# Kernel optimization log

Hardware: AMD Instinct MI355X
Metric: run time of the kernel (lower is better)

Reference implementation:

```python
import jax, jax.numpy as jnp
import numpy as np

HEADS = 16
DIM_HEAD = 64
EPS = 1e-5

def layer_norm(x, g, b):
    mu = jnp.mean(x, axis=-1, keepdims=True)
    var = jnp.mean(jnp.square(x - mu), axis=-1, keepdims=True)
    return (x - mu) * jax.lax.rsqrt(var + EPS) * g + b

def setup_inputs() -> dict:
    key = jax.random.key(0)
    ks = jax.random.split(key, 8)
    b, n_t, n_a = 4, 1024, 1024
    text_dim, audio_dim = 1024, 1024
    inner = HEADS * DIM_HEAD  # 1024
    s_in = 1.0 / np.sqrt(audio_dim)
    return {
        "text": jax.random.normal(ks[0], (b, n_t, text_dim), jnp.float32),
        "audio": jax.random.normal(ks[1], (b, n_a, audio_dim), jnp.float32),
        "g_text": jnp.ones((text_dim,), jnp.float32),
        "b_text": jnp.zeros((text_dim,), jnp.float32),
        "g_audio": jnp.ones((audio_dim,), jnp.float32),
        "b_audio": jnp.zeros((audio_dim,), jnp.float32),
        "W_qk": jax.random.normal(ks[2], (audio_dim, inner), jnp.float32) * s_in,
        "W_v": jax.random.normal(ks[3], (text_dim, inner), jnp.float32) * s_in,
        "W_out": jax.random.normal(ks[4], (inner, audio_dim), jnp.float32) * s_in,
        "b_out": jnp.zeros((audio_dim,), jnp.float32),
        "W_th": jax.random.normal(ks[5], (HEADS, HEADS), jnp.float32) / np.sqrt(HEADS),
    }

def reference(text, audio, g_text, b_text, g_audio, b_audio, W_qk, W_v, W_out, b_out, W_th):
    b = audio.shape[0]
    scale = DIM_HEAD ** -0.5
    text = layer_norm(text, g_text, b_text)
    audio = layer_norm(audio, g_audio, b_audio)
    # projections; qk acts as query, v acts as BOTH key and value
    qk = (audio @ W_qk).reshape(b, -1, HEADS, DIM_HEAD).transpose(0, 2, 1, 3)  # b h i d
    v = (text @ W_v).reshape(b, -1, HEADS, DIM_HEAD).transpose(0, 2, 1, 3)    # b h j d
    sim = jnp.einsum('bhid,bhjd->bhij', qk, v) * scale
    attn = jax.nn.softmax(sim, axis=-1)
    # talking-heads: 1x1 conv over head dim == mixing matrix over h
    attn = jnp.einsum('hg,bgij->bhij', W_th, attn)
    out = jnp.einsum('bhij,bhjd->bhid', attn, v)
    out = out.transpose(0, 2, 1, 3).reshape(b, -1, HEADS * DIM_HEAD)
    return out @ W_out + b_out
```

## Files before the change

kernel.cpp:

```cpp
#include <hip/hip_runtime.h>

typedef unsigned short u16;
typedef __bf16 bf16x8 __attribute__((ext_vector_type(8)));
typedef float f32x4 __attribute__((ext_vector_type(4)));
typedef unsigned short u16x4 __attribute__((ext_vector_type(4)));

static __device__ __forceinline__ u16 f2bf(float f){
  __bf16 h = (__bf16)f;
  return __builtin_bit_cast(u16, h);
}

#define MFMA(a,b,c) __builtin_amdgcn_mfma_f32_16x16x32_bf16(a,b,c,0,0,0)

__global__ __launch_bounds__(256) void ln_rows(const float* __restrict__ x,
    const float* __restrict__ g, const float* __restrict__ bta, u16* __restrict__ y)
{
  const int row = blockIdx.x;
  const int t = threadIdx.x;
  const float4 xv = ((const float4*)(x + (size_t)row*1024))[t];
  float s  = xv.x+xv.y+xv.z+xv.w;
  float sq = xv.x*xv.x+xv.y*xv.y+xv.z*xv.z+xv.w*xv.w;
  #pragma unroll
  for (int off=32; off; off>>=1){ s += __shfl_xor(s,off); sq += __shfl_xor(sq,off); }
  __shared__ float red[8];
  const int wid = t>>6, lane = t&63;
  if (lane==0){ red[wid]=s; red[4+wid]=sq; }
  __syncthreads();
  s  = red[0]+red[1]+red[2]+red[3];
  sq = red[4]+red[5]+red[6]+red[7];
  const float mu = s*(1.0f/1024.0f);
  float var = sq*(1.0f/1024.0f) - mu*mu;
  var = fmaxf(var, 0.0f);
  const float rs = rsqrtf(var + 1e-5f);
  const float4 gv = ((const float4*)g)[t];
  const float4 bv = ((const float4*)bta)[t];
  u16x4 o;
  o[0] = f2bf((xv.x-mu)*rs*gv.x + bv.x);
  o[1] = f2bf((xv.y-mu)*rs*gv.y + bv.y);
  o[2] = f2bf((xv.z-mu)*rs*gv.z + bv.z);
  o[3] = f2bf((xv.w-mu)*rs*gv.w + bv.w);
  ((u16x4*)(y + (size_t)row*1024))[t] = o;
}

__global__ __launch_bounds__(256) void transpose_w(const float* __restrict__ W, u16* __restrict__ WT)
{
  __shared__ float tile[32][33];
  const int tid = threadIdx.x;
  const int r0 = blockIdx.y*32, c0 = blockIdx.x*32;
  #pragma unroll
  for (int i=0;i<4;++i){
    int idx = i*256+tid; int r = idx>>5, c = idx&31;
    tile[r][c] = W[(size_t)(r0+r)*1024 + c0+c];
  }
  __syncthreads();
  #pragma unroll
  for (int i=0;i<4;++i){
    int idx = i*256+tid; int r = idx>>5, c = idx&31;
    WT[(size_t)(c0+r)*1024 + r0+c] = f2bf(tile[c][r]);
  }
}

__global__ __launch_bounds__(256) void transpose_v(const u16* __restrict__ V, u16* __restrict__ VT)
{
  __shared__ u16 tile[32][33];
  const int tid = threadIdx.x;
  const size_t base = (size_t)blockIdx.z * 1048576;
  const int r0 = blockIdx.y*32, c0 = blockIdx.x*32;
  #pragma unroll
  for (int i=0;i<4;++i){
    int idx = i*256+tid; int r = idx>>5, c = idx&31;
    tile[r][c] = V[base + (size_t)(r0+r)*1024 + c0+c];
  }
  __syncthreads();
  #pragma unroll
  for (int i=0;i<4;++i){
    int idx = i*256+tid; int r = idx>>5, c = idx&31;
    VT[base + (size_t)(c0+r)*1024 + r0+c] = tile[c][r];
  }
}

__global__ __launch_bounds__(256) void gemm_bt(const u16* __restrict__ A,
    const u16* __restrict__ Bt, u16* __restrict__ Cb, float* __restrict__ Cf,
    const float* __restrict__ bias, int outf)
{
  __shared__ u16 As[128][72];
  __shared__ u16 Bs[128][72];
  const int tid = threadIdx.x, lane = tid&63, wid = tid>>6;
  const int l15 = lane&15, l4 = lane>>4;
  const int m0 = blockIdx.y*128, n0 = blockIdx.x*128;
  const int wr = wid>>1, wc = wid&1;
  const int srow = tid>>3, scol = (tid&7)*8;
  const u16* Ag = A  + (size_t)(m0+srow)*1024 + scol;
  const u16* Bg = Bt + (size_t)(n0+srow)*1024 + scol;
  f32x4 acc[4][4];
  #pragma unroll
  for (int mt=0;mt<4;++mt)
    #pragma unroll
    for (int nt=0;nt<4;++nt) acc[mt][nt] = f32x4{0,0,0,0};

  for (int kt=0; kt<16; ++kt){
    const int k0 = kt*64;
    #pragma unroll
    for (int it=0; it<4; ++it){
      *(bf16x8*)&As[srow+it*32][scol] = *(const bf16x8*)(Ag + (size_t)it*32*1024 + k0);
      *(bf16x8*)&Bs[srow+it*32][scol] = *(const bf16x8*)(Bg + (size_t)it*32*1024 + k0);
    }
    __syncthreads();
    #pragma unroll
    for (int kk=0; kk<2; ++kk){
      bf16x8 af[4], bfv[4];
      #pragma unroll
      for (int mt=0;mt<4;++mt) af[mt]  = *(const bf16x8*)&As[wr*64+mt*16+l15][kk*32+8*l4];
      #pragma unroll
      for (int nt=0;nt<4;++nt) bfv[nt] = *(const bf16x8*)&Bs[wc*64+nt*16+l15][kk*32+8*l4];
      #pragma unroll
      for (int mt=0;mt<4;++mt)
        #pragma unroll
        for (int nt=0;nt<4;++nt)
          acc[mt][nt] = MFMA(af[mt], bfv[nt], acc[mt][nt]);
    }
    __syncthreads();
  }
  #pragma unroll
  for (int mt=0;mt<4;++mt)
    #pragma unroll
    for (int nt=0;nt<4;++nt)
      #pragma unroll
      for (int r=0;r<4;++r){
        const int row = m0 + wr*64+mt*16+l4*4+r;
        const int col = n0 + wc*64+nt*16+l15;
        if (outf) Cf[(size_t)row*1024+col] = acc[mt][nt][r] + bias[col];
        else      Cb[(size_t)row*1024+col] = f2bf(acc[mt][nt][r]);
      }
}

__global__ __launch_bounds__(256) void attn_stats(const u16* __restrict__ qk,
    const u16* __restrict__ v, float* __restrict__ m_arr, float* __restrict__ l_arr)
{
  const int lane = threadIdx.x & 63, wid = threadIdx.x >> 6;
  const int l15 = lane&15, l4 = lane>>4;
  const int b = blockIdx.z, g = blockIdx.y;
  const int i_base = blockIdx.x*64 + wid*16;
  const u16* qrow = qk + (size_t)(b*1024 + i_base + l15)*1024 + g*64 + 8*l4;
  const bf16x8 a0 = *(const bf16x8*)(qrow);
  const bf16x8 a1 = *(const bf16x8*)(qrow + 32);
  float mx[4] = {-1e30f,-1e30f,-1e30f,-1e30f};
  float sm[4] = {0.f,0.f,0.f,0.f};
  const u16* vbase = v + (size_t)(b*1024 + l15)*1024 + g*64 + 8*l4;
  for (int jt=0; jt<64; ++jt){
    const u16* vrow = vbase + (size_t)jt*16*1024;
    f32x4 c = {0,0,0,0};
    c = MFMA(a0, *(const bf16x8*)(vrow),      c);
    c = MFMA(a1, *(const bf16x8*)(vrow + 32), c);
    #pragma unroll
    for (int r=0;r<4;++r){
      const float s = c[r]*0.125f;
      const float nm = fmaxf(mx[r], s);
      sm[r] = sm[r]*__expf(mx[r]-nm) + __expf(s-nm);
      mx[r] = nm;
    }
  }
  #pragma unroll
  for (int r=0;r<4;++r){
    #pragma unroll
    for (int msk=1; msk<16; msk<<=1){
      const float om = __shfl_xor(mx[r], msk);
      const float os = __shfl_xor(sm[r], msk);
      const float nm = fmaxf(mx[r], om);
      sm[r] = sm[r]*__expf(mx[r]-nm) + os*__expf(om-nm);
      mx[r] = nm;
    }
  }
  if (l15 == 0){
    #pragma unroll
    for (int r=0;r<4;++r){
      const int i = i_base + l4*4 + r;
      const size_t idx = (size_t)(b*16+g)*1024 + i;
      m_arr[idx] = mx[r];
      l_arr[idx] = sm[r];
    }
  }
}

__global__ __launch_bounds__(256) void attn_mix_pv(const u16* __restrict__ qk,
    const u16* __restrict__ v, const u16* __restrict__ vt,
    const float* __restrict__ m_arr, const float* __restrict__ l_arr,
    const float* __restrict__ Wth, u16* __restrict__ attn_out)
{
  __shared__ float wth[256];
  __shared__ float P[16][16][36];
  const int tid = threadIdx.x;
  const int lane = tid&63, wid = tid>>6;
  const int l15 = lane&15, l4 = lane>>4;
  const int b = blockIdx.y;
  const int i0 = blockIdx.x*16;
  wth[tid] = Wth[tid];
  float mxs[4][4], ils[4][4];
  #pragma unroll
  for (int gg=0; gg<4; ++gg){
    const int g = wid*4+gg;
    #pragma unroll
    for (int r=0;r<4;++r){
      const size_t idx = (size_t)(b*16+g)*1024 + i0 + l4*4 + r;
      mxs[gg][r] = m_arr[idx];
      ils[gg][r] = 1.0f / l_arr[idx];
    }
  }
  bf16x8 aq[4][2];
  #pragma unroll
  for (int gg=0; gg<4; ++gg){
    const u16* qrow = qk + (size_t)(b*1024 + i0 + l15)*1024 + (wid*4+gg)*64 + 8*l4;
    aq[gg][0] = *(const bf16x8*)(qrow);
    aq[gg][1] = *(const bf16x8*)(qrow + 32);
  }
  f32x4 accO[4][4];
  #pragma unroll
  for (int hh=0;hh<4;++hh)
    #pragma unroll
    for (int dt=0;dt<4;++dt) accO[hh][dt] = f32x4{0,0,0,0};
  __syncthreads();

  for (int jt=0; jt<32; ++jt){
    const int j0 = jt*32;
    #pragma unroll
    for (int gg=0; gg<4; ++gg){
      const int g = wid*4+gg;
      #pragma unroll
      for (int jh=0; jh<2; ++jh){
        const u16* vrow = v + (size_t)(b*1024 + j0 + jh*16 + l15)*1024 + g*64 + 8*l4;
        f32x4 c = {0,0,0,0};
        c = MFMA(aq[gg][0], *(const bf16x8*)(vrow),      c);
        c = MFMA(aq[gg][1], *(const bf16x8*)(vrow + 32), c);
        #pragma unroll
        for (int r=0;r<4;++r){
          const float p = __expf(c[r]*0.125f - mxs[gg][r]) * ils[gg][r];
          P[g][l4*4+r][jh*16+l15] = p;
        }
      }
    }
    __syncthreads();
    float bh[4][8];
    #pragma unroll
    for (int hh=0;hh<4;++hh)
      #pragma unroll
      for (int e=0;e<8;++e) bh[hh][e] = 0.f;
    #pragma unroll
    for (int g2=0; g2<16; ++g2){
      const f32x4 p0 = *(const f32x4*)&P[g2][l15][8*l4];
      const f32x4 p1 = *(const f32x4*)&P[g2][l15][8*l4+4];
      #pragma unroll
      for (int hh=0; hh<4; ++hh){
        const float w = wth[(wid*4+hh)*16+g2];
        #pragma unroll
        for (int e=0;e<4;++e){ bh[hh][e] += w*p0[e]; bh[hh][4+e] += w*p1[e]; }
      }
    }
    #pragma unroll
    for (int hh=0; hh<4; ++hh){
      bf16x8 bfrag;
      #pragma unroll
      for (int e=0;e<8;++e) bfrag[e] = (__bf16)bh[hh][e];
      #pragma unroll
      for (int dt=0; dt<4; ++dt){
        const int c = (wid*4+hh)*64 + dt*16 + l15;
        const u16* vtrow = vt + (size_t)b*1048576 + (size_t)c*1024 + j0 + 8*l4;
        accO[hh][dt] = MFMA(bfrag, *(const bf16x8*)(vtrow), accO[hh][dt]);
      }
    }
    __syncthreads();
  }
  #pragma unroll
  for (int hh=0; hh<4; ++hh)
    #pragma unroll
    for (int dt=0; dt<4; ++dt)
      #pragma unroll
      for (int r=0;r<4;++r){
        const int i = i0 + l4*4 + r;
        const int col = (wid*4+hh)*64 + dt*16 + l15;
        attn_out[(size_t)(b*1024+i)*1024 + col] = f2bf(accO[hh][dt][r]);
      }
}

extern "C" void kernel_launch(void* const* d_in, const int* in_sizes, int n_in,
                              void* d_out, int out_size, void* d_ws, size_t ws_size,
                              hipStream_t stream) {
  const float* text    = (const float*)d_in[0];
  const float* audio   = (const float*)d_in[1];
  const float* g_text  = (const float*)d_in[2];
  const float* b_text  = (const float*)d_in[3];
  const float* g_audio = (const float*)d_in[4];
  const float* b_audio = (const float*)d_in[5];
  const float* W_qk    = (const float*)d_in[6];
  const float* W_v     = (const float*)d_in[7];
  const float* W_out   = (const float*)d_in[8];
  const float* b_out   = (const float*)d_in[9];
  const float* W_th    = (const float*)d_in[10];

  char* ws = (char*)d_ws;
  const size_t MB = 1024*1024;
  u16* text_n  = (u16*)(ws + 0*MB);
  u16* audio_n = (u16*)(ws + 8*MB);
  u16* WqkT    = (u16*)(ws + 16*MB);
  u16* WvT     = (u16*)(ws + 18*MB);
  u16* WoutT   = (u16*)(ws + 20*MB);
  u16* qk      = (u16*)(ws + 22*MB);
  u16* v       = (u16*)(ws + 30*MB);
  u16* vt      = (u16*)(ws + 38*MB);
  float* m_arr = (float*)(ws + 46*MB);
  float* l_arr = (float*)(ws + 47*MB);
  u16* attn_o  = (u16*)(ws + 48*MB);

  transpose_w<<<dim3(32,32), 256, 0, stream>>>(W_qk,  WqkT);
  transpose_w<<<dim3(32,32), 256, 0, stream>>>(W_v,   WvT);
  transpose_w<<<dim3(32,32), 256, 0, stream>>>(W_out, WoutT);
  ln_rows<<<4096, 256, 0, stream>>>(text,  g_text,  b_text,  text_n);
  ln_rows<<<4096, 256, 0, stream>>>(audio, g_audio, b_audio, audio_n);
  gemm_bt<<<dim3(8,32), 256, 0, stream>>>(audio_n, WqkT, qk, nullptr, nullptr, 0);
  gemm_bt<<<dim3(8,32), 256, 0, stream>>>(text_n,  WvT,  v,  nullptr, nullptr, 0);
  transpose_v<<<dim3(32,32,4), 256, 0, stream>>>(v, vt);
  attn_stats<<<dim3(16,16,4), 256, 0, stream>>>(qk, v, m_arr, l_arr);
  attn_mix_pv<<<dim3(64,4), 256, 0, stream>>>(qk, v, vt, m_arr, l_arr, W_th, attn_o);
  gemm_bt<<<dim3(8,32), 256, 0, stream>>>(attn_o, WoutT, nullptr, (float*)d_out, b_out, 1);
}
```

Before: 332.0 us.

## Split attention mix/PV over key chunks with 512-thread blocks and reduction pass

The fused attention-mix/PV kernel now uses 512 threads per block, two heads per wave, and optionally splits the key dimension into four chunks along grid z. Each chunk writes fp32 partial outputs that a new reduce kernel sums and converts to bf16. The goal is more blocks and waves in flight than the original 256-block grid, which underfills the GPU. The cost is extra fp32 partial traffic, an extra launch, and workspace buffers reassigned depending on available workspace size.

```diff
diff --git a/kernel.cpp b/kernel.cpp
--- a/kernel.cpp
+++ b/kernel.cpp
@@ -182,103 +182,106 @@
   }
 }
 
-__global__ __launch_bounds__(256) void attn_mix_pv(const u16* __restrict__ qk,
+__global__ __launch_bounds__(512,4) void attn_mix_pv2(const u16* __restrict__ qk,
     const u16* __restrict__ v, const u16* __restrict__ vt,
     const float* __restrict__ m_arr, const float* __restrict__ l_arr,
-    const float* __restrict__ Wth, u16* __restrict__ attn_out)
+    const float* __restrict__ Wth, float* __restrict__ Upart, int njt)
 {
   __shared__ float wth[256];
   __shared__ float P[16][16][36];
   const int tid = threadIdx.x;
   const int lane = tid&63, wid = tid>>6;
   const int l15 = lane&15, l4 = lane>>4;
-  const int b = blockIdx.y;
+  const int b = blockIdx.y, z = blockIdx.z;
   const int i0 = blockIdx.x*16;
-  wth[tid] = Wth[tid];
-  float mxs[4][4], ils[4][4];
-  #pragma unroll
-  for (int gg=0; gg<4; ++gg){
-    const int g = wid*4+gg;
+  const size_t bb = (size_t)b*1048576;
+  if (tid < 256) wth[tid] = Wth[tid];
+
+  float mxs[2][4], ils[2][4];
+  bf16x8 aq[2][2];
+  #pragma unroll
+  for (int gg=0; gg<2; ++gg){
+    const int g = 2*wid+gg;
     #pragma unroll
     for (int r=0;r<4;++r){
-      const size_t idx = (size_t)(b*16+g)*1024 + i0 + l4*4 + r;
+      const size_t idx = (size_t)(b*16+g)*1024 + i0 + 4*l4 + r;
       mxs[gg][r] = m_arr[idx];
       ils[gg][r] = 1.0f / l_arr[idx];
     }
-  }
-  bf16x8 aq[4][2];
-  #pragma unroll
-  for (int gg=0; gg<4; ++gg){
-    const u16* qrow = qk + (size_t)(b*1024 + i0 + l15)*1024 + (wid*4+gg)*64 + 8*l4;
-    aq[gg][0] = *(const bf16x8*)(qrow);
-    aq[gg][1] = *(const bf16x8*)(qrow + 32);
-  }
-  f32x4 accO[4][4];
-  #pragma unroll
-  for (int hh=0;hh<4;++hh)
-    #pragma unroll
-    for (int dt=0;dt<4;++dt) accO[hh][dt] = f32x4{0,0,0,0};
-  __syncthreads();
-
-  for (int jt=0; jt<32; ++jt){
-    const int j0 = jt*32;
-    #pragma unroll
-    for (int gg=0; gg<4; ++gg){
-      const int g = wid*4+gg;
+    const u16* qrow = qk + bb + (size_t)(i0+l15)*1024 + g*64 + 8*l4;
+    aq[gg][0] = *(const bf16x8*)qrow;
+    aq[gg][1] = *(const bf16x8*)(qrow+32);
+  }
+  f32x4 acc[2][4];
+  #pragma unroll
+  for (int hh=0;hh<2;++hh)
+    #pragma unroll
+    for (int dt=0;dt<4;++dt) acc[hh][dt] = f32x4{0,0,0,0};
+
+  for (int jt=0; jt<njt; ++jt){
+    const int j0 = (z*njt + jt)*32;
+    #pragma unroll
+    for (int gg=0; gg<2; ++gg){
+      const int g = 2*wid+gg;
       #pragma unroll
       for (int jh=0; jh<2; ++jh){
-        const u16* vrow = v + (size_t)(b*1024 + j0 + jh*16 + l15)*1024 + g*64 + 8*l4;
+        const u16* vrow = v + bb + (size_t)(j0 + jh*16 + l15)*1024 + g*64 + 8*l4;
         f32x4 c = {0,0,0,0};
         c = MFMA(aq[gg][0], *(const bf16x8*)(vrow),      c);
         c = MFMA(aq[gg][1], *(const bf16x8*)(vrow + 32), c);
         #pragma unroll
-        for (int r=0;r<4;++r){
-          const float p = __expf(c[r]*0.125f - mxs[gg][r]) * ils[gg][r];
-          P[g][l4*4+r][jh*16+l15] = p;
-        }
+        for (int r=0;r<4;++r)
+          P[g][4*l4+r][jh*16+l15] = __expf(c[r]*0.125f - mxs[gg][r]) * ils[gg][r];
       }
     }
     __syncthreads();
-    float bh[4][8];
-    #pragma unroll
-    for (int hh=0;hh<4;++hh)
-      #pragma unroll
-      for (int e=0;e<8;++e) bh[hh][e] = 0.f;
-    #pragma unroll
-    for (int g2=0; g2<16; ++g2){
-      const f32x4 p0 = *(const f32x4*)&P[g2][l15][8*l4];
-      const f32x4 p1 = *(const f32x4*)&P[g2][l15][8*l4+4];
-      #pragma unroll
-      for (int hh=0; hh<4; ++hh){
-        const float w = wth[(wid*4+hh)*16+g2];
+    #pragma unroll
+    for (int hh=0; hh<2; ++hh){
+      const int h = 2*wid+hh;
+      float bh[8];
+      #pragma unroll
+      for (int e=0;e<8;++e) bh[e] = 0.f;
+      #pragma unroll
+      for (int g2=0; g2<16; ++g2){
+        const f32x4 p0 = *(const f32x4*)&P[g2][l15][8*l4];
+        const f32x4 p1 = *(const f32x4*)&P[g2][l15][8*l4+4];
+        const float w = wth[h*16+g2];
         #pragma unroll
-        for (int e=0;e<4;++e){ bh[hh][e] += w*p0[e]; bh[hh][4+e] += w*p1[e]; }
+        for (int e=0;e<4;++e){ bh[e] += w*p0[e]; bh[4+e] += w*p1[e]; }
       }
-    }
-    #pragma unroll
-    for (int hh=0; hh<4; ++hh){
-      bf16x8 bfrag;
-      #pragma unroll
-      for (int e=0;e<8;++e) bfrag[e] = (__bf16)bh[hh][e];
-      #pragma unroll
-      for (int dt=0; dt<4; ++dt){
-        const int c = (wid*4+hh)*64 + dt*16 + l15;
-        const u16* vtrow = vt + (size_t)b*1048576 + (size_t)c*1024 + j0 + 8*l4;
-        accO[hh][dt] = MFMA(bfrag, *(const bf16x8*)(vtrow), accO[hh][dt]);
+      bf16x8 pf;
+      #pragma unroll
+      for (int e=0;e<8;++e) pf[e] = (__bf16)bh[e];
+      const u16* vtr = vt + bb + (size_t)(h*64 + l15)*1024 + j0 + 8*l4;
+      #pragma unroll
+      for (int dt=0; dt<4; ++dt)
+        acc[hh][dt] = MFMA(pf, *(const bf16x8*)(vtr + (size_t)dt*16*1024), acc[hh][dt]);
+    }
+    __syncthreads();
+  }
+  #pragma unroll
+  for (int hh=0; hh<2; ++hh)
+    #pragma unroll
+    for (int dt=0; dt<4; ++dt)
+      #pragma unroll
+      for (int r=0;r<4;++r){
+        const size_t row = (size_t)z*4096 + b*1024 + i0 + 4*l4 + r;
+        Upart[row*1024 + (2*wid+hh)*64 + dt*16 + l15] = acc[hh][dt][r];
       }
-    }
-    __syncthreads();
-  }
-  #pragma unroll
-  for (int hh=0; hh<4; ++hh)
-    #pragma unroll
-    for (int dt=0; dt<4; ++dt)
-      #pragma unroll
-      for (int r=0;r<4;++r){
-        const int i = i0 + l4*4 + r;
-        const int col = (wid*4+hh)*64 + dt*16 + l15;
-        attn_out[(size_t)(b*1024+i)*1024 + col] = f2bf(accO[hh][dt][r]);
-      }
+}
+
+__global__ __launch_bounds__(256) void reduce_u(const float* __restrict__ Upart,
+    u16* __restrict__ attn_o, int jc)
+{
+  const int row = blockIdx.x;
+  const int t = threadIdx.x;
+  f32x4 s = *(const f32x4*)(Upart + (size_t)row*1024 + 4*t);
+  for (int z=1; z<jc; ++z)
+    s += *(const f32x4*)(Upart + ((size_t)z*4096 + row)*1024 + 4*t);
+  u16x4 o;
+  #pragma unroll
+  for (int e=0;e<4;++e) o[e] = f2bf(s[e]);
+  *(u16x4*)(attn_o + (size_t)row*1024 + 4*t) = o;
 }
 
 extern "C" void kernel_launch(void* const* d_in, const int* in_sizes, int n_in,
@@ -306,9 +309,14 @@
   u16* qk      = (u16*)(ws + 22*MB);
   u16* v       = (u16*)(ws + 30*MB);
   u16* vt      = (u16*)(ws + 38*MB);
-  float* m_arr = (float*)(ws + 46*MB);
-  float* l_arr = (float*)(ws + 47*MB);
-  u16* attn_o  = (u16*)(ws + 48*MB);
+  float* m_arr = (float*)(ws + 16*MB);
+  float* l_arr = (float*)(ws + 16*MB + 256*1024);
+
+  const int jc = (ws_size >= 110*MB) ? 4 : 1;
+  float* Upart;
+  u16* attn_o;
+  if (jc == 4){ Upart = (float*)(ws + 46*MB); attn_o = (u16*)(ws + 0*MB); }
+  else        { Upart = (float*)(ws + 0*MB);  attn_o = (u16*)(ws + 46*MB); }
 
   transpose_w<<<dim3(32,32), 256, 0, stream>>>(W_qk,  WqkT);
   transpose_w<<<dim3(32,32), 256, 0, stream>>>(W_v,   WvT);
@@ -319,6 +327,7 @@
   gemm_bt<<<dim3(8,32), 256, 0, stream>>>(text_n,  WvT,  v,  nullptr, nullptr, 0);
   transpose_v<<<dim3(32,32,4), 256, 0, stream>>>(v, vt);
   attn_stats<<<dim3(16,16,4), 256, 0, stream>>>(qk, v, m_arr, l_arr);
-  attn_mix_pv<<<dim3(64,4), 256, 0, stream>>>(qk, v, vt, m_arr, l_arr, W_th, attn_o);
+  attn_mix_pv2<<<dim3(64,4,jc), 512, 0, stream>>>(qk, v, vt, m_arr, l_arr, W_th, Upart, 32/jc);
+  reduce_u<<<4096, 256, 0, stream>>>(Upart, attn_o, jc);
   gemm_bt<<<dim3(8,32), 256, 0, stream>>>(attn_o, WoutT, nullptr, (float*)d_out, b_out, 1);
 }
```

Measured after the change: 314.5 us. 1.06x faster.
